# Kernel tuning notes

Measured on AMD Instinct MI355X. Metric: run time of the kernel, lower is better.

Reference implementation:

```python
import jax, jax.numpy as jnp
import numpy as np

N_NODES = 50000


def sage_conv(x, edge_index, W_l, b_l, W_r):
    # PyG SAGEConv (mean aggr): out_i = lin_l(mean_{j->i} x_j) + lin_r(x_i)
    src, dst = edge_index[0], edge_index[1]
    msgs = x[src]                                        # [E, C] gather
    summed = jax.ops.segment_sum(msgs, dst, num_segments=N_NODES)  # [N, C]
    deg = jax.ops.segment_sum(jnp.ones((edge_index.shape[1],), x.dtype), dst,
                              num_segments=N_NODES)
    mean = summed / jnp.maximum(deg, 1.0)[:, None]
    return mean @ W_l + b_l + x @ W_r


def setup_inputs() -> dict:
    key = jax.random.key(0)
    ks = jax.random.split(key, 12)
    E, EL, C, X = 800000, 1000000, 128, 384
    return {
        "x": jax.random.normal(ks[0], (N_NODES, X), jnp.float32),
        "edge_index": jax.random.randint(ks[1], (2, E), 0, N_NODES),
        "edge_label_index": jax.random.randint(ks[2], (2, EL), 0, N_NODES),
        "W_lin": jax.random.normal(ks[3], (X, C), jnp.float32) * 0.05,
        "b_lin": jax.random.normal(ks[4], (C,), jnp.float32) * 0.05,
        "W1_l": jax.random.normal(ks[5], (C, C), jnp.float32) * 0.08,
        "b1": jax.random.normal(ks[6], (C,), jnp.float32) * 0.05,
        "W1_r": jax.random.normal(ks[7], (C, C), jnp.float32) * 0.08,
        "W2_l": jax.random.normal(ks[8], (C, C), jnp.float32) * 0.08,
        "b2": jax.random.normal(ks[9], (C,), jnp.float32) * 0.05,
        "W2_r": jax.random.normal(ks[10], (C, C), jnp.float32) * 0.08,
    }


def reference(x, edge_index, edge_label_index, W_lin, b_lin,
              W1_l, b1, W1_r, W2_l, b2, W2_r):
    h = x @ W_lin + b_lin                                # label_lin
    h = jax.nn.relu(sage_conv(h, edge_index, W1_l, b1, W1_r))
    h = sage_conv(h, edge_index, W2_l, b2, W2_r)
    # Classifier: dot product of head/tail node features per label edge
    head = h[edge_label_index[0]]
    tail = h[edge_label_index[1]]
    return (head * tail).sum(axis=-1)                    # [EL]
```

## Files before the change

kernel.cpp:

```cpp
#include <hip/hip_runtime.h>

#define NODES 50000
#define CH 128
#define ELLW 64

using frag_ab = __attribute__((ext_vector_type(8))) short;
using frag_cd = __attribute__((ext_vector_type(4))) float;

__device__ __forceinline__ float bf2f(ushort u) {
    union { unsigned u; float f; } v; v.u = ((unsigned)u) << 16; return v.f;
}
__device__ __forceinline__ ushort f2bf(float f) {
    union { float f; unsigned u; } v; v.f = f;
    unsigned r = v.u + 0x7fff + ((v.u >> 16) & 1);
    return (ushort)(r >> 16);
}

__global__ void prep_weights(const float* __restrict__ Wlin,
                             const float* __restrict__ W1l, const float* __restrict__ W1r,
                             const float* __restrict__ W2l, const float* __restrict__ W2r,
                             ushort* __restrict__ o0, ushort* __restrict__ o1,
                             ushort* __restrict__ o2, ushort* __restrict__ o3,
                             ushort* __restrict__ o4, int* __restrict__ deg) {
    int b = blockIdx.x;
    if (b >= 448) {
        int i = (b - 448) * 256 + threadIdx.y * 128 + threadIdx.x;
        if (i < NODES) deg[i] = 0;
        return;
    }
    const float* W; ushort* O; int K; int kb;
    if (b < 192) { W = Wlin; O = o0; K = 384; kb = b; }
    else {
        int j = (b - 192) >> 6; kb = (b - 192) & 63; K = 128;
        W = (j == 0) ? W1l : (j == 1) ? W1r : (j == 2) ? W2l : W2r;
        O = (j == 0) ? o1  : (j == 1) ? o2  : (j == 2) ? o3  : o4;
    }
    int k = kb * 2 + threadIdx.y;
    int n = threadIdx.x;
    if (k < K) O[(size_t)n * K + k] = f2bf(W[(size_t)k * 128 + n]);
}

__global__ void fill_ell(const int* __restrict__ ei, int E,
                         int* __restrict__ deg, int* __restrict__ ell) {
    int e = blockIdx.x * blockDim.x + threadIdx.x;
    if (e < E) {
        int d = ei[E + e];
        int pos = atomicAdd(&deg[d], 1);
        if (pos < ELLW) ell[(size_t)d * ELLW + pos] = ei[e];
    }
}

__global__ __launch_bounds__(256) void aggregate_ell(
    const ushort* __restrict__ h, const int* __restrict__ ell,
    const int* __restrict__ deg, ushort* __restrict__ mean, int N) {
    int node = blockIdx.x * 4 + (threadIdx.x >> 6);
    if (node >= N) return;
    int lane = threadIdx.x & 63;
    int g = lane >> 4;
    int q = lane & 15;
    const int* row = ell + (size_t)node * ELLW;
    int d = deg[node];
    int dc = d < ELLW ? d : ELLW;

    float acc[8];
#pragma unroll
    for (int k = 0; k < 8; ++k) acc[k] = 0.f;

    int n = 0;
    for (; n + 8 <= dc; n += 8) {
        int i0 = row[n + g];
        int i1 = row[n + 4 + g];
        uint4 v0 = *(const uint4*)(h + (size_t)i0 * CH + q * 8);
        uint4 v1 = *(const uint4*)(h + (size_t)i1 * CH + q * 8);
        acc[0] += bf2f((ushort)(v0.x & 0xffff)); acc[1] += bf2f((ushort)(v0.x >> 16));
        acc[2] += bf2f((ushort)(v0.y & 0xffff)); acc[3] += bf2f((ushort)(v0.y >> 16));
        acc[4] += bf2f((ushort)(v0.z & 0xffff)); acc[5] += bf2f((ushort)(v0.z >> 16));
        acc[6] += bf2f((ushort)(v0.w & 0xffff)); acc[7] += bf2f((ushort)(v0.w >> 16));
        acc[0] += bf2f((ushort)(v1.x & 0xffff)); acc[1] += bf2f((ushort)(v1.x >> 16));
        acc[2] += bf2f((ushort)(v1.y & 0xffff)); acc[3] += bf2f((ushort)(v1.y >> 16));
        acc[4] += bf2f((ushort)(v1.z & 0xffff)); acc[5] += bf2f((ushort)(v1.z >> 16));
        acc[6] += bf2f((ushort)(v1.w & 0xffff)); acc[7] += bf2f((ushort)(v1.w >> 16));
    }
    for (; n < dc; n += 4) {
        int j = n + g;
        if (j < dc) {
            int i0 = row[j];
            uint4 v0 = *(const uint4*)(h + (size_t)i0 * CH + q * 8);
            acc[0] += bf2f((ushort)(v0.x & 0xffff)); acc[1] += bf2f((ushort)(v0.x >> 16));
            acc[2] += bf2f((ushort)(v0.y & 0xffff)); acc[3] += bf2f((ushort)(v0.y >> 16));
            acc[4] += bf2f((ushort)(v0.z & 0xffff)); acc[5] += bf2f((ushort)(v0.z >> 16));
            acc[6] += bf2f((ushort)(v0.w & 0xffff)); acc[7] += bf2f((ushort)(v0.w >> 16));
        }
    }
#pragma unroll
    for (int k = 0; k < 8; ++k) {
        acc[k] += __shfl_xor(acc[k], 16, 64);
        acc[k] += __shfl_xor(acc[k], 32, 64);
    }
    if (g == 0) {
        float inv = 1.f / fmaxf((float)d, 1.f);
        uint4 o;
        o.x = ((uint)f2bf(acc[1] * inv) << 16) | (uint)f2bf(acc[0] * inv);
        o.y = ((uint)f2bf(acc[3] * inv) << 16) | (uint)f2bf(acc[2] * inv);
        o.z = ((uint)f2bf(acc[5] * inv) << 16) | (uint)f2bf(acc[4] * inv);
        o.w = ((uint)f2bf(acc[7] * inv) << 16) | (uint)f2bf(acc[6] * inv);
        *(uint4*)(mean + (size_t)node * CH + q * 8) = o;
    }
}

__global__ __launch_bounds__(256) void gemm_lin(
    const float* __restrict__ A, const ushort* __restrict__ Wt,
    const float* __restrict__ bias, ushort* __restrict__ out, int N)
{
    __shared__ ushort As[128 * 32];
    __shared__ ushort Bs[128 * 32];
    const int tid = threadIdx.x;
    const int lane = tid & 63;
    const int wave = tid >> 6;
    const int wr = wave >> 1, wc = wave & 1;
    const int row0 = blockIdx.x * 128;
    const int l15 = lane & 15, quad = lane >> 4;

    frag_cd acc[4][4];
#pragma unroll
    for (int i = 0; i < 4; ++i)
#pragma unroll
        for (int j = 0; j < 4; ++j) acc[i][j] = (frag_cd){0.f, 0.f, 0.f, 0.f};

#pragma unroll 1
    for (int k0 = 0; k0 < 384; k0 += 32) {
        __syncthreads();
#pragma unroll
        for (int i = 0; i < 4; ++i) {
            int e = i * 256 + tid;
            int r = e >> 3, q = e & 7;
            int gr = row0 + r; if (gr > N - 1) gr = N - 1;
            float4 v = *(const float4*)(A + (size_t)gr * 384 + k0 + q * 4);
            ushort4 o; o.x = f2bf(v.x); o.y = f2bf(v.y); o.z = f2bf(v.z); o.w = f2bf(v.w);
            *(ushort4*)(As + r * 32 + q * 4) = o;
        }
#pragma unroll
        for (int i = 0; i < 2; ++i) {
            int e = i * 256 + tid;
            int nn = e >> 2, kq = e & 3;
            uint4 v = *(const uint4*)(Wt + (size_t)nn * 384 + k0 + kq * 8);
            *(uint4*)(Bs + e * 8) = v;
        }
        __syncthreads();

        frag_ab a[4], b[4];
#pragma unroll
        for (int i = 0; i < 4; ++i)
            a[i] = *(const frag_ab*)(As + (wr * 64 + i * 16 + l15) * 32 + quad * 8);
#pragma unroll
        for (int j = 0; j < 4; ++j)
            b[j] = *(const frag_ab*)(Bs + (wc * 64 + j * 16 + l15) * 32 + quad * 8);
#pragma unroll
        for (int i = 0; i < 4; ++i)
#pragma unroll
            for (int j = 0; j < 4; ++j)
                acc[i][j] = __builtin_amdgcn_mfma_f32_16x16x32_bf16(a[i], b[j], acc[i][j], 0, 0, 0);
    }

#pragma unroll
    for (int i = 0; i < 4; ++i)
#pragma unroll
        for (int r = 0; r < 4; ++r) {
            int row = row0 + wr * 64 + i * 16 + quad * 4 + r;
            if (row < N)
#pragma unroll
                for (int j = 0; j < 4; ++j) {
                    int col = wc * 64 + j * 16 + l15;
                    out[(size_t)row * 128 + col] = f2bf(acc[i][j][r] + bias[col]);
                }
        }
}

template <bool RELU>
__global__ __launch_bounds__(256) void mfma_gemm(
    const ushort* __restrict__ A1, const ushort* __restrict__ Wt1,
    const ushort* __restrict__ A2, const ushort* __restrict__ Wt2,
    const float* __restrict__ bias, ushort* __restrict__ out, int N)
{
    __shared__ ushort As[128 * 32];
    __shared__ ushort Bs[128 * 32];
    const int tid = threadIdx.x;
    const int lane = tid & 63;
    const int wave = tid >> 6;
    const int wr = wave >> 1, wc = wave & 1;
    const int row0 = blockIdx.x * 128;
    const int l15 = lane & 15, quad = lane >> 4;

    frag_cd acc[4][4];
#pragma unroll
    for (int i = 0; i < 4; ++i)
#pragma unroll
        for (int j = 0; j < 4; ++j) acc[i][j] = (frag_cd){0.f, 0.f, 0.f, 0.f};

#pragma unroll 1
    for (int part = 0; part < 2; ++part) {
        const ushort* A  = part ? A2 : A1;
        const ushort* Wt = part ? Wt2 : Wt1;

#pragma unroll 1
        for (int k0 = 0; k0 < 128; k0 += 32) {
            __syncthreads();
#pragma unroll
            for (int i = 0; i < 2; ++i) {
                int e = i * 256 + tid;
                int r = e >> 2, kq = e & 3;
                int gr = row0 + r; if (gr > N - 1) gr = N - 1;
                uint4 v = *(const uint4*)(A + (size_t)gr * 128 + k0 + kq * 8);
                *(uint4*)(As + e * 8) = v;
            }
#pragma unroll
            for (int i = 0; i < 2; ++i) {
                int e = i * 256 + tid;
                int nn = e >> 2, kq = e & 3;
                uint4 v = *(const uint4*)(Wt + (size_t)nn * 128 + k0 + kq * 8);
                *(uint4*)(Bs + e * 8) = v;
            }
            __syncthreads();

            frag_ab a[4], b[4];
#pragma unroll
            for (int i = 0; i < 4; ++i)
                a[i] = *(const frag_ab*)(As + (wr * 64 + i * 16 + l15) * 32 + quad * 8);
#pragma unroll
            for (int j = 0; j < 4; ++j)
                b[j] = *(const frag_ab*)(Bs + (wc * 64 + j * 16 + l15) * 32 + quad * 8);
#pragma unroll
            for (int i = 0; i < 4; ++i)
#pragma unroll
                for (int j = 0; j < 4; ++j)
                    acc[i][j] = __builtin_amdgcn_mfma_f32_16x16x32_bf16(a[i], b[j], acc[i][j], 0, 0, 0);
        }
    }

#pragma unroll
    for (int i = 0; i < 4; ++i)
#pragma unroll
        for (int r = 0; r < 4; ++r) {
            int row = row0 + wr * 64 + i * 16 + quad * 4 + r;
            if (row < N)
#pragma unroll
                for (int j = 0; j < 4; ++j) {
                    int col = wc * 64 + j * 16 + l15;
                    float v = acc[i][j][r] + bias[col];
                    if (RELU) v = fmaxf(v, 0.f);
                    out[(size_t)row * 128 + col] = f2bf(v);
                }
        }
}

__device__ __forceinline__ float dot8(uint4 va, uint4 vb) {
    float p = 0.f;
    p += bf2f((ushort)(va.x & 0xffff)) * bf2f((ushort)(vb.x & 0xffff));
    p += bf2f((ushort)(va.x >> 16))    * bf2f((ushort)(vb.x >> 16));
    p += bf2f((ushort)(va.y & 0xffff)) * bf2f((ushort)(vb.y & 0xffff));
    p += bf2f((ushort)(va.y >> 16))    * bf2f((ushort)(vb.y >> 16));
    p += bf2f((ushort)(va.z & 0xffff)) * bf2f((ushort)(vb.z & 0xffff));
    p += bf2f((ushort)(va.z >> 16))    * bf2f((ushort)(vb.z >> 16));
    p += bf2f((ushort)(va.w & 0xffff)) * bf2f((ushort)(vb.w & 0xffff));
    p += bf2f((ushort)(va.w >> 16))    * bf2f((ushort)(vb.w >> 16));
    return p;
}

__global__ __launch_bounds__(256) void classify_bf(
    const ushort* __restrict__ h2, const int* __restrict__ eli,
    int EL, float* __restrict__ out) {
    int gt = blockIdx.x * blockDim.x + threadIdx.x;
    int g0 = (gt >> 4) * 4;
    int lane = gt & 15;
    if (g0 >= EL) return;
    bool full = (g0 + 3 < EL);
    int4 ha, ta;
    if (full) {
        ha = *(const int4*)(eli + g0);
        ta = *(const int4*)(eli + EL + g0);
    } else {
        int e1 = g0 + 1 < EL ? g0 + 1 : g0;
        int e2 = g0 + 2 < EL ? g0 + 2 : g0;
        ha = make_int4(eli[g0], eli[e1], eli[e2], eli[e2]);
        ta = make_int4(eli[EL + g0], eli[EL + e1], eli[EL + e2], eli[EL + e2]);
    }
    uint4 va0 = *((const uint4*)(h2 + (size_t)ha.x * CH) + lane);
    uint4 vb0 = *((const uint4*)(h2 + (size_t)ta.x * CH) + lane);
    uint4 va1 = *((const uint4*)(h2 + (size_t)ha.y * CH) + lane);
    uint4 vb1 = *((const uint4*)(h2 + (size_t)ta.y * CH) + lane);
    uint4 va2 = *((const uint4*)(h2 + (size_t)ha.z * CH) + lane);
    uint4 vb2 = *((const uint4*)(h2 + (size_t)ta.z * CH) + lane);
    uint4 va3 = *((const uint4*)(h2 + (size_t)ha.w * CH) + lane);
    uint4 vb3 = *((const uint4*)(h2 + (size_t)ta.w * CH) + lane);
    float p0 = dot8(va0, vb0);
    float p1 = dot8(va1, vb1);
    float p2 = dot8(va2, vb2);
    float p3 = dot8(va3, vb3);
#pragma unroll
    for (int s = 8; s >= 1; s >>= 1) {
        p0 += __shfl_down(p0, s, 16);
        p1 += __shfl_down(p1, s, 16);
        p2 += __shfl_down(p2, s, 16);
        p3 += __shfl_down(p3, s, 16);
    }
    if (lane == 0) {
        if (full) {
            *(float4*)(out + g0) = make_float4(p0, p1, p2, p3);
        } else {
            out[g0] = p0;
            if (g0 + 1 < EL) out[g0 + 1] = p1;
            if (g0 + 2 < EL) out[g0 + 2] = p2;
        }
    }
}

extern "C" void kernel_launch(void* const* d_in, const int* in_sizes, int n_in,
                              void* d_out, int out_size, void* d_ws, size_t ws_size,
                              hipStream_t stream) {
    const float* x     = (const float*)d_in[0];
    const int*   ei    = (const int*)d_in[1];
    const int*   eli   = (const int*)d_in[2];
    const float* W_lin = (const float*)d_in[3];
    const float* b_lin = (const float*)d_in[4];
    const float* W1l   = (const float*)d_in[5];
    const float* b1    = (const float*)d_in[6];
    const float* W1r   = (const float*)d_in[7];
    const float* W2l   = (const float*)d_in[8];
    const float* b2    = (const float*)d_in[9];
    const float* W2r   = (const float*)d_in[10];
    float* out = (float*)d_out;

    const int E  = in_sizes[1] / 2;
    const int EL = in_sizes[2] / 2;
    const int N  = NODES;

    char* ws = (char*)d_ws;
    size_t off = 0;
    auto alloc = [&](size_t bytes) -> void* {
        void* p = ws + off;
        off += (bytes + 255) & ~(size_t)255;
        return p;
    };
    ushort* n0    = (ushort*)alloc((size_t)N * CH * sizeof(ushort));
    ushort* n1    = (ushort*)alloc((size_t)N * CH * sizeof(ushort));
    ushort* n2    = (ushort*)alloc((size_t)N * CH * sizeof(ushort));
    ushort* WtLin = (ushort*)alloc((size_t)CH * 384 * sizeof(ushort));
    ushort* Wt1l  = (ushort*)alloc((size_t)CH * CH * sizeof(ushort));
    ushort* Wt1r  = (ushort*)alloc((size_t)CH * CH * sizeof(ushort));
    ushort* Wt2l  = (ushort*)alloc((size_t)CH * CH * sizeof(ushort));
    ushort* Wt2r  = (ushort*)alloc((size_t)CH * CH * sizeof(ushort));
    int* deg = (int*)alloc((size_t)N * sizeof(int));
    int* ell = (int*)alloc((size_t)N * ELLW * sizeof(int));
    (void)ws_size; (void)n_in; (void)out_size;

    prep_weights<<<dim3(644), dim3(128, 2), 0, stream>>>(
        W_lin, W1l, W1r, W2l, W2r, WtLin, Wt1l, Wt1r, Wt2l, Wt2r, deg);

    fill_ell<<<dim3((E + 255) / 256), dim3(256), 0, stream>>>(ei, E, deg, ell);

    const int gblocks = (N + 127) / 128;
    const int ablocks = (N + 3) / 4;

    gemm_lin<<<dim3(gblocks), dim3(256), 0, stream>>>(x, WtLin, b_lin, n0, N);

    aggregate_ell<<<dim3(ablocks), dim3(256), 0, stream>>>(n0, ell, deg, n1, N);
    mfma_gemm<true><<<dim3(gblocks), dim3(256), 0, stream>>>(
        n1, Wt1l, n0, Wt1r, b1, n2, N);

    aggregate_ell<<<dim3(ablocks), dim3(256), 0, stream>>>(n2, ell, deg, n1, N);
    mfma_gemm<false><<<dim3(gblocks), dim3(256), 0, stream>>>(
        n1, Wt2l, n2, Wt2r, b2, n0, N);

    long long groups = ((long long)EL + 3) / 4;
    long long cls_threads = groups * 16;
    classify_bf<<<dim3((int)((cls_threads + 255) / 256)), dim3(256), 0, stream>>>(
        n0, eli, EL, out);
}
```

Before: 330.2 us.

## Fuse pipeline stages into one cooperative persistent kernel with grid syncs

Replaces the seven separate launches (weight prep, ELL fill, input linear, two aggregate+GEMM pairs) with a single cooperative persistent kernel that loops over tiles per stage and separates stages with grid.sync. The aim is to remove kernel launch gaps and per-launch tail effects. In exchange, the grid is capped at 1024 blocks, which limits occupancy and load balance. Each stage also now waits on a full grid barrier, and the GEMM tiles gain an extra block barrier.

```diff
diff --git a/kernel.cpp b/kernel.cpp
--- a/kernel.cpp
+++ b/kernel.cpp
@@ -1,4 +1,7 @@
 #include <hip/hip_runtime.h>
+#include <hip/hip_cooperative_groups.h>
+
+namespace cg = cooperative_groups;
 
 #define NODES 50000
 #define CH 128
@@ -16,44 +19,11 @@
     return (ushort)(r >> 16);
 }
 
-__global__ void prep_weights(const float* __restrict__ Wlin,
-                             const float* __restrict__ W1l, const float* __restrict__ W1r,
-                             const float* __restrict__ W2l, const float* __restrict__ W2r,
-                             ushort* __restrict__ o0, ushort* __restrict__ o1,
-                             ushort* __restrict__ o2, ushort* __restrict__ o3,
-                             ushort* __restrict__ o4, int* __restrict__ deg) {
-    int b = blockIdx.x;
-    if (b >= 448) {
-        int i = (b - 448) * 256 + threadIdx.y * 128 + threadIdx.x;
-        if (i < NODES) deg[i] = 0;
-        return;
-    }
-    const float* W; ushort* O; int K; int kb;
-    if (b < 192) { W = Wlin; O = o0; K = 384; kb = b; }
-    else {
-        int j = (b - 192) >> 6; kb = (b - 192) & 63; K = 128;
-        W = (j == 0) ? W1l : (j == 1) ? W1r : (j == 2) ? W2l : W2r;
-        O = (j == 0) ? o1  : (j == 1) ? o2  : (j == 2) ? o3  : o4;
-    }
-    int k = kb * 2 + threadIdx.y;
-    int n = threadIdx.x;
-    if (k < K) O[(size_t)n * K + k] = f2bf(W[(size_t)k * 128 + n]);
-}
-
-__global__ void fill_ell(const int* __restrict__ ei, int E,
-                         int* __restrict__ deg, int* __restrict__ ell) {
-    int e = blockIdx.x * blockDim.x + threadIdx.x;
-    if (e < E) {
-        int d = ei[E + e];
-        int pos = atomicAdd(&deg[d], 1);
-        if (pos < ELLW) ell[(size_t)d * ELLW + pos] = ei[e];
-    }
-}
-
-__global__ __launch_bounds__(256) void aggregate_ell(
-    const ushort* __restrict__ h, const int* __restrict__ ell,
-    const int* __restrict__ deg, ushort* __restrict__ mean, int N) {
-    int node = blockIdx.x * 4 + (threadIdx.x >> 6);
+
+__device__ void agg4(const ushort* __restrict__ h, const int* __restrict__ ell,
+                     const int* __restrict__ deg, ushort* __restrict__ mean,
+                     int N, int grp) {
+    int node = grp * 4 + (threadIdx.x >> 6);
     if (node >= N) return;
     int lane = threadIdx.x & 63;
     int g = lane >> 4;
@@ -108,17 +78,13 @@
     }
 }
 
-__global__ __launch_bounds__(256) void gemm_lin(
-    const float* __restrict__ A, const ushort* __restrict__ Wt,
-    const float* __restrict__ bias, ushort* __restrict__ out, int N)
-{
-    __shared__ ushort As[128 * 32];
-    __shared__ ushort Bs[128 * 32];
+__device__ void gemm_lin_tile(const float* __restrict__ A, const ushort* __restrict__ Wt,
+                              const float* __restrict__ bias, ushort* __restrict__ out,
+                              int N, int row0, ushort* As, ushort* Bs) {
     const int tid = threadIdx.x;
     const int lane = tid & 63;
     const int wave = tid >> 6;
     const int wr = wave >> 1, wc = wave & 1;
-    const int row0 = blockIdx.x * 128;
     const int l15 = lane & 15, quad = lane >> 4;
 
     frag_cd acc[4][4];
@@ -142,8 +108,7 @@
 #pragma unroll
         for (int i = 0; i < 2; ++i) {
             int e = i * 256 + tid;
-            int nn = e >> 2, kq = e & 3;
-            uint4 v = *(const uint4*)(Wt + (size_t)nn * 384 + k0 + kq * 8);
+            uint4 v = *(const uint4*)(Wt + (size_t)(e >> 2) * 384 + k0 + (e & 3) * 8);
             *(uint4*)(Bs + e * 8) = v;
         }
         __syncthreads();
@@ -161,6 +126,7 @@
             for (int j = 0; j < 4; ++j)
                 acc[i][j] = __builtin_amdgcn_mfma_f32_16x16x32_bf16(a[i], b[j], acc[i][j], 0, 0, 0);
     }
+    __syncthreads();
 
 #pragma unroll
     for (int i = 0; i < 4; ++i)
@@ -176,19 +142,14 @@
         }
 }
 
-template <bool RELU>
-__global__ __launch_bounds__(256) void mfma_gemm(
-    const ushort* __restrict__ A1, const ushort* __restrict__ Wt1,
-    const ushort* __restrict__ A2, const ushort* __restrict__ Wt2,
-    const float* __restrict__ bias, ushort* __restrict__ out, int N)
-{
-    __shared__ ushort As[128 * 32];
-    __shared__ ushort Bs[128 * 32];
+__device__ void gemm_tile_dual(const ushort* __restrict__ A1, const ushort* __restrict__ Wt1,
+                               const ushort* __restrict__ A2, const ushort* __restrict__ Wt2,
+                               const float* __restrict__ bias, ushort* __restrict__ out,
+                               int N, int row0, bool relu, ushort* As, ushort* Bs) {
     const int tid = threadIdx.x;
     const int lane = tid & 63;
     const int wave = tid >> 6;
     const int wr = wave >> 1, wc = wave & 1;
-    const int row0 = blockIdx.x * 128;
     const int l15 = lane & 15, quad = lane >> 4;
 
     frag_cd acc[4][4];
@@ -201,7 +162,6 @@
     for (int part = 0; part < 2; ++part) {
         const ushort* A  = part ? A2 : A1;
         const ushort* Wt = part ? Wt2 : Wt1;
-
 #pragma unroll 1
         for (int k0 = 0; k0 < 128; k0 += 32) {
             __syncthreads();
@@ -216,8 +176,7 @@
 #pragma unroll
             for (int i = 0; i < 2; ++i) {
                 int e = i * 256 + tid;
-                int nn = e >> 2, kq = e & 3;
-                uint4 v = *(const uint4*)(Wt + (size_t)nn * 128 + k0 + kq * 8);
+                uint4 v = *(const uint4*)(Wt + (size_t)(e >> 2) * 128 + k0 + (e & 3) * 8);
                 *(uint4*)(Bs + e * 8) = v;
             }
             __syncthreads();
@@ -236,6 +195,7 @@
                     acc[i][j] = __builtin_amdgcn_mfma_f32_16x16x32_bf16(a[i], b[j], acc[i][j], 0, 0, 0);
         }
     }
+    __syncthreads();
 
 #pragma unroll
     for (int i = 0; i < 4; ++i)
@@ -247,10 +207,79 @@
                 for (int j = 0; j < 4; ++j) {
                     int col = wc * 64 + j * 16 + l15;
                     float v = acc[i][j][r] + bias[col];
-                    if (RELU) v = fmaxf(v, 0.f);
+                    if (relu) v = fmaxf(v, 0.f);
                     out[(size_t)row * 128 + col] = f2bf(v);
                 }
         }
+}
+
+
+struct MegaArgs {
+    const float* x; const int* ei;
+    const float* Wlin; const float* blin;
+    const float* W1l; const float* b1; const float* W1r;
+    const float* W2l; const float* b2; const float* W2r;
+    ushort *n0, *n1, *n2, *WtLin, *Wt1l, *Wt1r, *Wt2l, *Wt2r;
+    int *deg, *ell;
+    int E, N;
+};
+
+__global__ __launch_bounds__(256, 4) void mega(MegaArgs a) {
+    __shared__ ushort As[128 * 32];
+    __shared__ ushort Bs[128 * 32];
+    cg::grid_group grid = cg::this_grid();
+    const int tid = threadIdx.x;
+    const int tstride = gridDim.x * 256;
+    const int gtiles = (a.N + 127) >> 7;
+    const int agroups = (a.N + 3) >> 2;
+
+    for (int i = blockIdx.x * 256 + tid; i < 114688 + a.N; i += tstride) {
+        if (i < 49152) {
+            int k = i >> 7, n = i & 127;
+            a.WtLin[(size_t)n * 384 + k] = f2bf(a.Wlin[i]);
+        } else if (i < 114688) {
+            int j = i - 49152; int m = j >> 14; int r = j & 16383;
+            int k = r >> 7, n = r & 127;
+            const float* W = (m == 0) ? a.W1l : (m == 1) ? a.W1r : (m == 2) ? a.W2l : a.W2r;
+            ushort* O      = (m == 0) ? a.Wt1l : (m == 1) ? a.Wt1r : (m == 2) ? a.Wt2l : a.Wt2r;
+            O[(size_t)n * 128 + k] = f2bf(W[r]);
+        } else {
+            a.deg[i - 114688] = 0;
+        }
+    }
+    __threadfence();
+    grid.sync();
+
+    for (int e = blockIdx.x * 256 + tid; e < a.E; e += tstride) {
+        int d = a.ei[a.E + e];
+        int pos = atomicAdd(&a.deg[d], 1);
+        if (pos < ELLW) a.ell[(size_t)d * ELLW + pos] = a.ei[e];
+    }
+    __threadfence();
+    grid.sync();
+
+    for (int t = blockIdx.x; t < gtiles; t += gridDim.x)
+        gemm_lin_tile(a.x, a.WtLin, a.blin, a.n0, a.N, t * 128, As, Bs);
+    __threadfence();
+    grid.sync();
+
+    for (int g = blockIdx.x; g < agroups; g += gridDim.x)
+        agg4(a.n0, a.ell, a.deg, a.n1, a.N, g);
+    __threadfence();
+    grid.sync();
+
+    for (int t = blockIdx.x; t < gtiles; t += gridDim.x)
+        gemm_tile_dual(a.n1, a.Wt1l, a.n0, a.Wt1r, a.b1, a.n2, a.N, t * 128, true, As, Bs);
+    __threadfence();
+    grid.sync();
+
+    for (int g = blockIdx.x; g < agroups; g += gridDim.x)
+        agg4(a.n2, a.ell, a.deg, a.n1, a.N, g);
+    __threadfence();
+    grid.sync();
+
+    for (int t = blockIdx.x; t < gtiles; t += gridDim.x)
+        gemm_tile_dual(a.n1, a.Wt2l, a.n2, a.Wt2r, a.b2, a.n0, a.N, t * 128, false, As, Bs);
 }
 
 __device__ __forceinline__ float dot8(uint4 va, uint4 vb) {
@@ -317,19 +346,6 @@
 extern "C" void kernel_launch(void* const* d_in, const int* in_sizes, int n_in,
                               void* d_out, int out_size, void* d_ws, size_t ws_size,
                               hipStream_t stream) {
-    const float* x     = (const float*)d_in[0];
-    const int*   ei    = (const int*)d_in[1];
-    const int*   eli   = (const int*)d_in[2];
-    const float* W_lin = (const float*)d_in[3];
-    const float* b_lin = (const float*)d_in[4];
-    const float* W1l   = (const float*)d_in[5];
-    const float* b1    = (const float*)d_in[6];
-    const float* W1r   = (const float*)d_in[7];
-    const float* W2l   = (const float*)d_in[8];
-    const float* b2    = (const float*)d_in[9];
-    const float* W2r   = (const float*)d_in[10];
-    float* out = (float*)d_out;
-
     const int E  = in_sizes[1] / 2;
     const int EL = in_sizes[2] / 2;
     const int N  = NODES;
@@ -353,26 +369,35 @@
     int* ell = (int*)alloc((size_t)N * ELLW * sizeof(int));
     (void)ws_size; (void)n_in; (void)out_size;
 
-    prep_weights<<<dim3(644), dim3(128, 2), 0, stream>>>(
-        W_lin, W1l, W1r, W2l, W2r, WtLin, Wt1l, Wt1r, Wt2l, Wt2r, deg);
-
-    fill_ell<<<dim3((E + 255) / 256), dim3(256), 0, stream>>>(ei, E, deg, ell);
-
-    const int gblocks = (N + 127) / 128;
-    const int ablocks = (N + 3) / 4;
-
-    gemm_lin<<<dim3(gblocks), dim3(256), 0, stream>>>(x, WtLin, b_lin, n0, N);
-
-    aggregate_ell<<<dim3(ablocks), dim3(256), 0, stream>>>(n0, ell, deg, n1, N);
-    mfma_gemm<true><<<dim3(gblocks), dim3(256), 0, stream>>>(
-        n1, Wt1l, n0, Wt1r, b1, n2, N);
-
-    aggregate_ell<<<dim3(ablocks), dim3(256), 0, stream>>>(n2, ell, deg, n1, N);
-    mfma_gemm<false><<<dim3(gblocks), dim3(256), 0, stream>>>(
-        n1, Wt2l, n2, Wt2r, b2, n0, N);
-
+    MegaArgs margs;
+    margs.x    = (const float*)d_in[0];
+    margs.ei   = (const int*)d_in[1];
+    margs.Wlin = (const float*)d_in[3];
+    margs.blin = (const float*)d_in[4];
+    margs.W1l  = (const float*)d_in[5];
+    margs.b1   = (const float*)d_in[6];
+    margs.W1r  = (const float*)d_in[7];
+    margs.W2l  = (const float*)d_in[8];
+    margs.b2   = (const float*)d_in[9];
+    margs.W2r  = (const float*)d_in[10];
+    margs.n0 = n0; margs.n1 = n1; margs.n2 = n2;
+    margs.WtLin = WtLin; margs.Wt1l = Wt1l; margs.Wt1r = Wt1r;
+    margs.Wt2l = Wt2l; margs.Wt2r = Wt2r;
+    margs.deg = deg; margs.ell = ell;
+    margs.E = E; margs.N = N;
+
+    int perCU = 0;
+    if (hipOccupancyMaxActiveBlocksPerMultiprocessor(&perCU, mega, 256, 0) != hipSuccess
+        || perCU < 1) perCU = 2;
+    int grid = perCU * 256;
+    if (grid > 1024) grid = 1024;
+
+    void* kargs[] = { (void*)&margs };
+    hipLaunchCooperativeKernel((const void*)mega, dim3(grid), dim3(256), kargs, 0, stream);
+
+    const int* eli = (const int*)d_in[2];
     long long groups = ((long long)EL + 3) / 4;
     long long cls_threads = groups * 16;
     classify_bf<<<dim3((int)((cls_threads + 255) / 256)), dim3(256), 0, stream>>>(
-        n0, eli, EL, out);
-}
+        n0, eli, EL, (float*)d_out);
+}
```

Measured after the change: 1.121 ms. 239% more time.
